# Optimization experiments

Hardware: AMD Instinct MI355X
Metric: run time of the kernel (lower is better)

Reference implementation:

```python
import jax, jax.numpy as jnp
import numpy as np

B, T, L = 256, 512, 40
VOCAB, ED, NC, H = 30000, 8, 22, 64
IN = ED + NC + 1  # GRUCell input: embed + cont + vanco feedback


def setup_inputs():
    key = jax.random.key(0)
    ks = jax.random.split(key, 10)
    cont = jax.random.uniform(ks[0], (B, T, NC), dtype=jnp.float32)
    cat = jax.random.randint(ks[1], (B, T, L), 0, VOCAB, dtype=jnp.int32)
    lb = jax.random.uniform(ks[2], (B, T), dtype=jnp.float32)
    mask = jax.random.randint(ks[3], (B, T), 0, 2, dtype=jnp.int32)
    d = jax.random.uniform(ks[4], (B, T), dtype=jnp.float32)
    td = jax.random.uniform(ks[5], (B, T), dtype=jnp.float32)
    emb = jax.random.normal(ks[6], (VOCAB, ED), dtype=jnp.float32) * 0.1
    emb = emb.at[0].set(0.0)  # padding_idx=0
    W_ih = jax.random.normal(ks[7], (3 * H, IN), dtype=jnp.float32) * 0.1
    W_hh = jax.random.normal(ks[8], (3 * H, H), dtype=jnp.float32) * 0.1
    b_ih = jnp.zeros((3 * H,), jnp.float32)
    b_hh = jnp.zeros((3 * H,), jnp.float32)
    W_out = jax.random.normal(ks[9], (4, H), dtype=jnp.float32) * 0.1
    b_out = jnp.zeros((4,), jnp.float32)
    return dict(cont=cont, cat=cat, lb=lb, mask=mask, d=d, td=td, emb=emb,
                W_ih=W_ih, W_hh=W_hh, b_ih=b_ih, b_hh=b_hh, W_out=W_out, b_out=b_out)


def _forward(cont, cat, lb, mask, d, td, emb, W_ih, W_hh, b_ih, b_hh, W_out, b_out):
    # demographic-derived creatinine clearance, exactly as in the torch code
    age = cont[:, :1, 2] * 16.936469 + 58.239251          # [B,1]
    weight = cont[:, :1, 21] * 30.519849 + 87.5752         # [B,1]
    creat = cont[..., 11] * 1.418099 + 1.314668            # [B,T]
    gender = (cat[:, :1, :] == 5).sum(2).astype(jnp.float32) * 0.15 + 0.85  # [B,1]
    ccl = (140.0 - age) * weight * gender / 72.0 / creat   # [B,T]
    # embedding sum over codes + continuous features
    outEmb = jnp.concatenate([emb[cat].sum(2), cont], axis=2)  # [B,T,ED+NC]
    td24 = td * 24.0
    mf = mask.astype(jnp.float32)
    # step i uses mask/lb of step i-1 for the vanco feedback (0 at i=0)
    mask_prev = jnp.concatenate([jnp.zeros_like(mf[:, :1]), mf[:, :-1]], axis=1)
    lb_prev = jnp.concatenate([jnp.zeros_like(lb[:, :1]), lb[:, :-1]], axis=1)
    Bn = cont.shape[0]

    def step(carry, x):
        h, C, D, A = carry
        e, mp, lp, cc, dd, tt = x
        vfb = jax.lax.stop_gradient(A) * (1.0 - mp) + lp * mp
        xi = jnp.concatenate([e, vfb[:, None]], axis=1)     # [B, IN]
        gi = xi @ W_ih.T + b_ih
        gh = h @ W_hh.T + b_hh
        ir, iz, inn = jnp.split(gi, 3, axis=1)
        hr, hz, hn = jnp.split(gh, 3, axis=1)
        r = jax.nn.sigmoid(ir + hr)
        z = jax.nn.sigmoid(iz + hz)
        n = jnp.tanh(inn + r * hn)
        h = (1.0 - z) * n + z * h                            # GRUCell update
        eta = h @ W_out.T + b_out                            # [B,4]
        e1, e2, e3, e4 = eta[:, 0], eta[:, 1], eta[:, 2], eta[:, 3]
        v1 = 33.1 * jnp.exp(e1)
        k1 = 3.96 * cc / 100.0 * jnp.exp(e2)
        rr = 1000.0 / v1
        v2 = 48.3 * jnp.exp(e4)
        R = -6.99 / 48.3 * jnp.exp(e3)
        k2 = R * v2
        delta = jnp.sqrt((k1 - k2 - R * v1) ** 2 + 4.0 * k1 * R * v1) / v1
        s = (-k1 + k2 + R * v1) / v1
        lam1 = (s - delta) / 2.0
        lam2 = (s + delta) / 2.0
        C1 = rr * (k2 / v1) / lam1 / delta
        C2 = -rr * (k2 / v1) / lam2 / delta
        C3 = -(lam1 - R) / (k2 / v1)
        C4 = -(lam2 - R) / (k2 / v1)
        Cn = ((C + C1) * jnp.exp(lam1 * dd) - C1) * jnp.exp(lam1 * (tt - dd))
        Dn = ((D + C2) * jnp.exp(lam2 * dd) - C2) * jnp.exp(lam2 * (tt - dd))
        An = Cn * C3 + Dn * C4
        return (h, Cn, Dn, An), An

    z0 = jnp.zeros((Bn,), jnp.float32)
    carry0 = (jnp.zeros((Bn, H), jnp.float32), z0, z0, z0)
    xs = (outEmb.transpose(1, 0, 2), mask_prev.T, lb_prev.T, ccl.T, d.T, td24.T)
    _, A_seq = jax.lax.scan(step, carry0, xs)
    return A_seq.T  # [B,T] predicted vancomycin concentration


def reference(cont, cat, lb, mask, d, td, emb, W_ih, W_hh, b_ih, b_hh, W_out, b_out):
    return _forward(cont, cat, lb, mask, d, td, emb, W_ih, W_hh, b_ih, b_hh, W_out, b_out)
```

## Files before the change

kernel.cpp:

```cpp
#include <hip/hip_runtime.h>
#include <math.h>

#define BB 256
#define TT 512
#define LL 40
#define ED 8
#define NC 22
#define HH 64
#define BLK 320

#define L2E 1.4426950408889634f
#define S2E 2.8853900817779268f

__device__ __forceinline__ float fast_rcp(float x)  { return __builtin_amdgcn_rcpf(x); }
__device__ __forceinline__ float fast_exp2(float x) { return __builtin_amdgcn_exp2f(x); }

__device__ __forceinline__ float dpp_add_xor1(float x) {
    int v = __builtin_amdgcn_update_dpp(0, __float_as_int(x), 0xB1, 0xF, 0xF, true);
    return x + __int_as_float(v);
}
__device__ __forceinline__ float dpp_add_xor2(float x) {
    int v = __builtin_amdgcn_update_dpp(0, __float_as_int(x), 0x4E, 0xF, 0xF, true);
    return x + __int_as_float(v);
}
__device__ __forceinline__ float quad_sum(float x) { return dpp_add_xor2(dpp_add_xor1(x)); }

__device__ __forceinline__ float dpp_reduce16(float x) {
    int v;
    v = __builtin_amdgcn_update_dpp(0, __float_as_int(x), 0xB1, 0xF, 0xF, true);  x += __int_as_float(v);
    v = __builtin_amdgcn_update_dpp(0, __float_as_int(x), 0x4E, 0xF, 0xF, true);  x += __int_as_float(v);
    v = __builtin_amdgcn_update_dpp(0, __float_as_int(x), 0x141, 0xF, 0xF, true); x += __int_as_float(v);
    v = __builtin_amdgcn_update_dpp(0, __float_as_int(x), 0x140, 0xF, 0xF, true); x += __int_as_float(v);
    return x;
}

__global__ __launch_bounds__(BLK, 1) void scan_kernel(
    const float* __restrict__ cont, const int* __restrict__ cat,
    const float* __restrict__ lb, const int* __restrict__ mask,
    const float* __restrict__ dvec, const float* __restrict__ td,
    const float* __restrict__ emb,
    const float* __restrict__ W_ih, const float* __restrict__ W_hh,
    const float* __restrict__ b_ih, const float* __restrict__ b_hh,
    const float* __restrict__ W_out, const float* __restrict__ b_out,
    float* __restrict__ out)
{
    const int b   = blockIdx.x;
    const int tid = threadIdx.x;

    __shared__ __align__(128) float  feat[TT * 32];
    __shared__ __align__(16)  float4 sc[TT];
    __shared__ float  cclA[TT];
    __shared__ __align__(128) float hbuf[72];
    __shared__ __align__(16) float out_lds[TT];
    __shared__ float vfb_lds;
    __shared__ float kb_lds;

    const size_t bT    = (size_t)b * TT;
    const int*   catb  = cat  + bT * LL;
    const float* contb = cont + bT * NC;

    const bool isDot = (tid >= 64);
    const int  Ld = tid - 64;
    const int  j  = Ld >> 2;
    const int  q  = Ld & 3;
    const int  ei = tid & 15, ej = tid >> 4;

    float wr_[24], wz_[24], wn_[24];
    float br = 0.f, bz = 0.f, bnx = 0.f, bnh = 0.f;
    float w30r = 0.f, w30z = 0.f, w30n = 0.f;
    float wo0 = 0.f, wo1 = 0.f, wo2 = 0.f, wo3 = 0.f;
    if (isDot) {
        #pragma unroll
        for (int m = 0; m < 24; ++m) {
            const int f = 24 * q + m;
            float a, c, d;
            if (f < 30)      { a = W_ih[j*31+f]; c = W_ih[(j+64)*31+f]; d = W_ih[(j+128)*31+f]; }
            else if (f < 32) { a = 0.f; c = 0.f; d = 0.f; }
            else             { a = W_hh[j*64+f-32]; c = W_hh[(j+64)*64+f-32]; d = W_hh[(j+128)*64+f-32]; }
            wr_[m] = a * L2E;
            wz_[m] = c * L2E;
            wn_[m] = d * S2E;
        }
        #pragma unroll
        for (int m = 0; m < 24; ++m) {
            asm volatile("" : "+v"(wr_[m]));
            asm volatile("" : "+v"(wz_[m]));
            asm volatile("" : "+v"(wn_[m]));
        }
        br   = (b_ih[j]      + b_hh[j])      * L2E;
        bz   = (b_ih[j + 64] + b_hh[j + 64]) * L2E;
        bnx  = b_ih[j + 128] * S2E;
        bnh  = b_hh[j + 128] * S2E;
        w30r = W_ih[j*31 + 30]        * L2E;
        w30z = W_ih[(j+64)*31 + 30]   * L2E;
        w30n = W_ih[(j+128)*31 + 30]  * S2E;
    } else {
        wo0 = W_out[ej * 64 + 4*ei + 0] * L2E;
        wo1 = W_out[ej * 64 + 4*ei + 1] * L2E;
        wo2 = W_out[ej * 64 + 4*ei + 2] * L2E;
        wo3 = W_out[ej * 64 + 4*ei + 3] * L2E;
    }
    const float boL0 = b_out[0] * L2E, boL1 = b_out[1] * L2E;
    const float boL2 = b_out[2] * L2E, boL3 = b_out[3] * L2E;

    for (int i = tid; i < TT * NC; i += BLK) {
        int r = i / NC, c = i - r * NC;
        feat[r * 32 + 8 + c] = contb[i];
    }
    for (int i = tid; i < TT; i += BLK) {
        feat[i * 32 + 30] = 0.f;
        feat[i * 32 + 31] = 0.f;
    }
    for (int i = tid; i < TT * 8; i += BLK) {
        int r = i >> 3, e = i & 7;
        const int* cp = catb + r * LL;
        float acc = 0.f;
        #pragma unroll 8
        for (int l = 0; l < LL; ++l) acc += emb[cp[l] * ED + e];
        feat[r * 32 + e] = acc;
    }
    for (int i = tid; i < TT; i += BLK) {
        float d   = dvec[bT + i];
        float t24 = td[bT + i] * 24.0f;
        sc[i] = make_float4(d * L2E, (t24 - d) * L2E, (float)mask[bT + i], lb[bT + i]);
    }
    if (tid < 72) hbuf[tid] = 0.f;
    if (tid == 0) vfb_lds = 0.f;
    if (tid < 64) {
        int cv = (tid < LL) ? catb[tid] : 0;
        unsigned long long bal = __ballot(tid < LL && cv == 5);
        float g   = (float)__popcll(bal) * 0.15f + 0.85f;
        float age = contb[2]  * 16.936469f + 58.239251f;
        float wgt = contb[21] * 30.519849f + 87.5752f;
        if (tid == 0) kb_lds = (140.0f - age) * wgt * g / 72.0f;
    }
    __syncthreads();
    {
        const float Kb = kb_lds;
        for (int i = tid; i < TT; i += BLK)
            cclA[i] = Kb * fast_rcp(fmaf(contb[i * NC + 11], 1.418099f, 1.314668f));
    }
    __syncthreads();

    float hreg = 0.f;
    float Cc = 0.f, Dc = 0.f;
    float sr = 0.f, sz = 0.f, snx = 0.f, snh = 0.f;
    float4 svc = make_float4(0.f, 0.f, 0.f, 0.f);
    float  ccv = 0.f;

    const float4* hA4 = (const float4*)hbuf;
    const float4* hB4 = (const float4*)(hbuf + 36);

    auto do_dots = [&](int t) {
        const float4* f4t = (const float4*)(feat + t * 32);
        float ra = 0.f, za = 0.f, nxa = 0.f, nha = 0.f;
        #pragma unroll
        for (int k = 0; k < 6; ++k) {
            const int idx = 6 * q + k;
            const float4* pH = (idx < 16) ? (hA4 + (idx - 8)) : (hB4 + (idx - 16));
            const float4* p  = (idx < 8) ? (f4t + idx) : pH;
            const float4 uv = *p;
            ra = fmaf(uv.x, wr_[4*k+0], ra);
            ra = fmaf(uv.y, wr_[4*k+1], ra);
            ra = fmaf(uv.z, wr_[4*k+2], ra);
            ra = fmaf(uv.w, wr_[4*k+3], ra);
            za = fmaf(uv.x, wz_[4*k+0], za);
            za = fmaf(uv.y, wz_[4*k+1], za);
            za = fmaf(uv.z, wz_[4*k+2], za);
            za = fmaf(uv.w, wz_[4*k+3], za);
            if (idx < 8) {
                nxa = fmaf(uv.x, wn_[4*k+0], nxa);
                nxa = fmaf(uv.y, wn_[4*k+1], nxa);
                nxa = fmaf(uv.z, wn_[4*k+2], nxa);
                nxa = fmaf(uv.w, wn_[4*k+3], nxa);
            } else {
                nha = fmaf(uv.x, wn_[4*k+0], nha);
                nha = fmaf(uv.y, wn_[4*k+1], nha);
                nha = fmaf(uv.z, wn_[4*k+2], nha);
                nha = fmaf(uv.w, wn_[4*k+3], nha);
            }
        }
        sr  = quad_sum(ra);
        sz  = quad_sum(za);
        snx = quad_sum(nxa);
        snh = quad_sum(nha);
    };

    if (isDot) do_dots(0);

    for (int t = 0; t < TT; ++t) {
        if (isDot) {
            const float vfb = vfb_lds;
            float prer = sr + br + vfb * w30r;
            float prez = sz + bz + vfb * w30z;
            float r = fast_rcp(1.0f + fast_exp2(-prer));
            float z = fast_rcp(1.0f + fast_exp2(-prez));
            float yp = snx + bnx + vfb * w30n + r * (snh + bnh);
            float n = 1.0f - 2.0f * fast_rcp(fast_exp2(yp) + 1.0f);
            hreg = fmaf(z, hreg - n, n);
            if (q == 0) hbuf[(j < 32) ? j : (36 + j - 32)] = hreg;
        } else {
            svc = sc[t];
            ccv = cclA[t];
        }
        __syncthreads();

        if (isDot) {
            if (t + 1 < TT) do_dots(t + 1);
        } else {
            const float4 hv = (ei < 8) ? hA4[ei] : hB4[ei - 8];
            float p = hv.x * wo0;
            p = fmaf(hv.y, wo1, p);
            p = fmaf(hv.z, wo2, p);
            p = fmaf(hv.w, wo3, p);
            p = dpp_reduce16(p);
            const float e0 = __int_as_float(__builtin_amdgcn_readlane(__float_as_int(p), 0));
            const float e1 = __int_as_float(__builtin_amdgcn_readlane(__float_as_int(p), 16));
            const float e2 = __int_as_float(__builtin_amdgcn_readlane(__float_as_int(p), 32));
            const float e3 = __int_as_float(__builtin_amdgcn_readlane(__float_as_int(p), 48));

            float E1 = fast_exp2(e0 + boL0);
            float E2 = fast_exp2(e1 + boL1);
            float E3 = fast_exp2(e2 + boL2);
            float E4 = fast_exp2(e3 + boL3);
            float v1  = 33.1f * E1;
            float rv1 = fast_rcp(v1);
            float k1  = 0.0396f * ccv * E2;
            float rrr = 1000.0f * rv1;
            float v2  = 48.3f * E4;
            float R   = (-6.99f / 48.3f) * E3;
            float k2  = R * v2;
            float qq  = k1 - k2 - R * v1;
            float disc = fmaf(qq, qq, 4.0f * k1 * R * v1);
            float delta = __builtin_amdgcn_sqrtf(disc) * rv1;
            float sgm  = (k2 - k1 + R * v1) * rv1;
            float lam1 = (sgm - delta) * 0.5f;
            float lam2 = (sgm + delta) * 0.5f;
            float kv  = k2 * rv1;
            float rkv = fast_rcp(kv);
            float C1  = rrr * kv * fast_rcp(lam1 * delta);
            float C2  = -rrr * kv * fast_rcp(lam2 * delta);
            float C3  = -(lam1 - R) * rkv;
            float C4  = -(lam2 - R) * rkv;
            float Cn  = fmaf(Cc + C1, fast_exp2(lam1 * svc.x), -C1) * fast_exp2(lam1 * svc.y);
            float Dn  = fmaf(Dc + C2, fast_exp2(lam2 * svc.x), -C2) * fast_exp2(lam2 * svc.y);
            float An  = fmaf(Cn, C3, Dn * C4);
            Cc = Cn; Dc = Dn;
            if (tid == 0) {
                out_lds[t] = An;
                vfb_lds = fmaf(An, 1.0f - svc.z, svc.w * svc.z);
            }
        }
        __syncthreads();
    }

    if (tid < TT / 4) ((float4*)(out + bT))[tid] = ((const float4*)out_lds)[tid];
}

extern "C" void kernel_launch(void* const* d_in, const int* in_sizes, int n_in,
                              void* d_out, int out_size, void* d_ws, size_t ws_size,
                              hipStream_t stream) {
    const float* cont  = (const float*)d_in[0];
    const int*   cat   = (const int*)  d_in[1];
    const float* lb    = (const float*)d_in[2];
    const int*   mask  = (const int*)  d_in[3];
    const float* dvec  = (const float*)d_in[4];
    const float* td    = (const float*)d_in[5];
    const float* emb   = (const float*)d_in[6];
    const float* W_ih  = (const float*)d_in[7];
    const float* W_hh  = (const float*)d_in[8];
    const float* b_ih  = (const float*)d_in[9];
    const float* b_hh  = (const float*)d_in[10];
    const float* W_out = (const float*)d_in[11];
    const float* b_out = (const float*)d_in[12];
    float* out = (float*)d_out;

    hipLaunchKernelGGL(scan_kernel, dim3(BB), dim3(BLK), 0, stream,
                       cont, cat, lb, mask, dvec, td, emb, W_ih, W_hh, b_ih, b_hh,
                       W_out, b_out, out);
}
```

Before: 476.1 us.

## Split each GRU row dot product across 8 lanes and widen block to 576

```diff
diff --git a/kernel.cpp b/kernel.cpp
--- a/kernel.cpp
+++ b/kernel.cpp
@@ -7,7 +7,7 @@
 #define ED 8
 #define NC 22
 #define HH 64
-#define BLK 320
+#define BLK 576
 
 #define L2E 1.4426950408889634f
 #define S2E 2.8853900817779268f
@@ -23,8 +23,13 @@
     int v = __builtin_amdgcn_update_dpp(0, __float_as_int(x), 0x4E, 0xF, 0xF, true);
     return x + __int_as_float(v);
 }
-__device__ __forceinline__ float quad_sum(float x) { return dpp_add_xor2(dpp_add_xor1(x)); }
-
+__device__ __forceinline__ float dpp_add_mirror8(float x) {
+    int v = __builtin_amdgcn_update_dpp(0, __float_as_int(x), 0x141, 0xF, 0xF, true);
+    return x + __int_as_float(v);
+}
+__device__ __forceinline__ float red8(float x) {
+    return dpp_add_mirror8(dpp_add_xor2(dpp_add_xor1(x)));
+}
 __device__ __forceinline__ float dpp_reduce16(float x) {
     int v;
     v = __builtin_amdgcn_update_dpp(0, __float_as_int(x), 0xB1, 0xF, 0xF, true);  x += __int_as_float(v);
@@ -34,7 +39,7 @@
     return x;
 }
 
-__global__ __launch_bounds__(BLK, 1) void scan_kernel(
+__global__ __launch_bounds__(BLK, 3) void scan_kernel(
     const float* __restrict__ cont, const int* __restrict__ cat,
     const float* __restrict__ lb, const int* __restrict__ mask,
     const float* __restrict__ dvec, const float* __restrict__ td,
@@ -50,8 +55,8 @@
     __shared__ __align__(128) float  feat[TT * 32];
     __shared__ __align__(16)  float4 sc[TT];
     __shared__ float  cclA[TT];
-    __shared__ __align__(128) float hbuf[72];
-    __shared__ __align__(16) float out_lds[TT];
+    __shared__ __align__(16)  float  hbuf[HH];
+    __shared__ __align__(16)  float  out_lds[TT];
     __shared__ float vfb_lds;
     __shared__ float kb_lds;
 
@@ -59,30 +64,36 @@
     const int*   catb  = cat  + bT * LL;
     const float* contb = cont + bT * NC;
 
-    const bool isDot = (tid >= 64);
-    const int  Ld = tid - 64;
-    const int  j  = Ld >> 2;
-    const int  q  = Ld & 3;
-    const int  ei = tid & 15, ej = tid >> 4;
-
-    float wr_[24], wz_[24], wn_[24];
+    const bool isDot = (tid < 512);
+    const int  j  = tid >> 3;
+    const int  s  = tid & 7;
+    const int  l8 = tid - 512;
+    const int  ei = l8 & 15, ej = l8 >> 4;
+
+    float wr_[12], wz_[12], wn_[12];
     float br = 0.f, bz = 0.f, bnx = 0.f, bnh = 0.f;
     float w30r = 0.f, w30z = 0.f, w30n = 0.f;
     float wo0 = 0.f, wo1 = 0.f, wo2 = 0.f, wo3 = 0.f;
     if (isDot) {
+        const int cx0 = 4 * s;
         #pragma unroll
-        for (int m = 0; m < 24; ++m) {
-            const int f = 24 * q + m;
-            float a, c, d;
-            if (f < 30)      { a = W_ih[j*31+f]; c = W_ih[(j+64)*31+f]; d = W_ih[(j+128)*31+f]; }
-            else if (f < 32) { a = 0.f; c = 0.f; d = 0.f; }
-            else             { a = W_hh[j*64+f-32]; c = W_hh[(j+64)*64+f-32]; d = W_hh[(j+128)*64+f-32]; }
-            wr_[m] = a * L2E;
-            wz_[m] = c * L2E;
-            wn_[m] = d * S2E;
+        for (int m = 0; m < 4; ++m) {
+            const int cx = cx0 + m;
+            const float xr = (cx < 30) ? W_ih[j * 31 + cx]         : 0.f;
+            const float xz = (cx < 30) ? W_ih[(j + 64) * 31 + cx]  : 0.f;
+            const float xn = (cx < 30) ? W_ih[(j + 128) * 31 + cx] : 0.f;
+            wr_[m]     = xr * L2E;
+            wz_[m]     = xz * L2E;
+            wn_[m]     = xn * S2E;
+            wr_[4 + m] = W_hh[j * 64 + cx]              * L2E;
+            wz_[4 + m] = W_hh[(j + 64) * 64 + cx]       * L2E;
+            wn_[4 + m] = W_hh[(j + 128) * 64 + cx]      * S2E;
+            wr_[8 + m] = W_hh[j * 64 + 32 + cx]         * L2E;
+            wz_[8 + m] = W_hh[(j + 64) * 64 + 32 + cx]  * L2E;
+            wn_[8 + m] = W_hh[(j + 128) * 64 + 32 + cx] * S2E;
         }
         #pragma unroll
-        for (int m = 0; m < 24; ++m) {
+        for (int m = 0; m < 12; ++m) {
             asm volatile("" : "+v"(wr_[m]));
             asm volatile("" : "+v"(wz_[m]));
             asm volatile("" : "+v"(wn_[m]));
@@ -91,14 +102,14 @@
         bz   = (b_ih[j + 64] + b_hh[j + 64]) * L2E;
         bnx  = b_ih[j + 128] * S2E;
         bnh  = b_hh[j + 128] * S2E;
-        w30r = W_ih[j*31 + 30]        * L2E;
-        w30z = W_ih[(j+64)*31 + 30]   * L2E;
-        w30n = W_ih[(j+128)*31 + 30]  * S2E;
+        w30r = W_ih[j * 31 + 30]         * L2E;
+        w30z = W_ih[(j + 64) * 31 + 30]  * L2E;
+        w30n = W_ih[(j + 128) * 31 + 30] * S2E;
     } else {
-        wo0 = W_out[ej * 64 + 4*ei + 0] * L2E;
-        wo1 = W_out[ej * 64 + 4*ei + 1] * L2E;
-        wo2 = W_out[ej * 64 + 4*ei + 2] * L2E;
-        wo3 = W_out[ej * 64 + 4*ei + 3] * L2E;
+        wo0 = W_out[ej * 64 + 4 * ei + 0] * L2E;
+        wo1 = W_out[ej * 64 + 4 * ei + 1] * L2E;
+        wo2 = W_out[ej * 64 + 4 * ei + 2] * L2E;
+        wo3 = W_out[ej * 64 + 4 * ei + 3] * L2E;
     }
     const float boL0 = b_out[0] * L2E, boL1 = b_out[1] * L2E;
     const float boL2 = b_out[2] * L2E, boL3 = b_out[3] * L2E;
@@ -111,20 +122,23 @@
         feat[i * 32 + 30] = 0.f;
         feat[i * 32 + 31] = 0.f;
     }
-    for (int i = tid; i < TT * 8; i += BLK) {
-        int r = i >> 3, e = i & 7;
+    for (int i = tid; i < TT * 2; i += BLK) {
+        int r = i >> 1, qd = i & 1;
         const int* cp = catb + r * LL;
-        float acc = 0.f;
+        float4 acc = make_float4(0.f, 0.f, 0.f, 0.f);
         #pragma unroll 8
-        for (int l = 0; l < LL; ++l) acc += emb[cp[l] * ED + e];
-        feat[r * 32 + e] = acc;
+        for (int l = 0; l < LL; ++l) {
+            const float4 ev = *((const float4*)(emb + cp[l] * ED) + qd);
+            acc.x += ev.x; acc.y += ev.y; acc.z += ev.z; acc.w += ev.w;
+        }
+        ((float4*)feat)[r * 8 + qd] = acc;
     }
     for (int i = tid; i < TT; i += BLK) {
         float d   = dvec[bT + i];
         float t24 = td[bT + i] * 24.0f;
         sc[i] = make_float4(d * L2E, (t24 - d) * L2E, (float)mask[bT + i], lb[bT + i]);
     }
-    if (tid < 72) hbuf[tid] = 0.f;
+    if (tid < HH) hbuf[tid] = 0.f;
     if (tid == 0) vfb_lds = 0.f;
     if (tid < 64) {
         int cv = (tid < LL) ? catb[tid] : 0;
@@ -148,42 +162,53 @@
     float4 svc = make_float4(0.f, 0.f, 0.f, 0.f);
     float  ccv = 0.f;
 
-    const float4* hA4 = (const float4*)hbuf;
-    const float4* hB4 = (const float4*)(hbuf + 36);
+    const float4* hbuf4 = (const float4*)hbuf;
 
     auto do_dots = [&](int t) {
-        const float4* f4t = (const float4*)(feat + t * 32);
-        float ra = 0.f, za = 0.f, nxa = 0.f, nha = 0.f;
-        #pragma unroll
-        for (int k = 0; k < 6; ++k) {
-            const int idx = 6 * q + k;
-            const float4* pH = (idx < 16) ? (hA4 + (idx - 8)) : (hB4 + (idx - 16));
-            const float4* p  = (idx < 8) ? (f4t + idx) : pH;
-            const float4 uv = *p;
-            ra = fmaf(uv.x, wr_[4*k+0], ra);
-            ra = fmaf(uv.y, wr_[4*k+1], ra);
-            ra = fmaf(uv.z, wr_[4*k+2], ra);
-            ra = fmaf(uv.w, wr_[4*k+3], ra);
-            za = fmaf(uv.x, wz_[4*k+0], za);
-            za = fmaf(uv.y, wz_[4*k+1], za);
-            za = fmaf(uv.z, wz_[4*k+2], za);
-            za = fmaf(uv.w, wz_[4*k+3], za);
-            if (idx < 8) {
-                nxa = fmaf(uv.x, wn_[4*k+0], nxa);
-                nxa = fmaf(uv.y, wn_[4*k+1], nxa);
-                nxa = fmaf(uv.z, wn_[4*k+2], nxa);
-                nxa = fmaf(uv.w, wn_[4*k+3], nxa);
-            } else {
-                nha = fmaf(uv.x, wn_[4*k+0], nha);
-                nha = fmaf(uv.y, wn_[4*k+1], nha);
-                nha = fmaf(uv.z, wn_[4*k+2], nha);
-                nha = fmaf(uv.w, wn_[4*k+3], nha);
-            }
-        }
-        sr  = quad_sum(ra);
-        sz  = quad_sum(za);
-        snx = quad_sum(nxa);
-        snh = quad_sum(nha);
+        const float4 u0 = ((const float4*)(feat + t * 32))[s];
+        const float4 u1 = hbuf4[s];
+        const float4 u2 = hbuf4[s + 8];
+        float ra, za, nxa, nha;
+        ra  = u0.x * wr_[0];
+        ra  = fmaf(u0.y, wr_[1],  ra);
+        ra  = fmaf(u0.z, wr_[2],  ra);
+        ra  = fmaf(u0.w, wr_[3],  ra);
+        ra  = fmaf(u1.x, wr_[4],  ra);
+        ra  = fmaf(u1.y, wr_[5],  ra);
+        ra  = fmaf(u1.z, wr_[6],  ra);
+        ra  = fmaf(u1.w, wr_[7],  ra);
+        ra  = fmaf(u2.x, wr_[8],  ra);
+        ra  = fmaf(u2.y, wr_[9],  ra);
+        ra  = fmaf(u2.z, wr_[10], ra);
+        ra  = fmaf(u2.w, wr_[11], ra);
+        za  = u0.x * wz_[0];
+        za  = fmaf(u0.y, wz_[1],  za);
+        za  = fmaf(u0.z, wz_[2],  za);
+        za  = fmaf(u0.w, wz_[3],  za);
+        za  = fmaf(u1.x, wz_[4],  za);
+        za  = fmaf(u1.y, wz_[5],  za);
+        za  = fmaf(u1.z, wz_[6],  za);
+        za  = fmaf(u1.w, wz_[7],  za);
+        za  = fmaf(u2.x, wz_[8],  za);
+        za  = fmaf(u2.y, wz_[9],  za);
+        za  = fmaf(u2.z, wz_[10], za);
+        za  = fmaf(u2.w, wz_[11], za);
+        nxa = u0.x * wn_[0];
+        nxa = fmaf(u0.y, wn_[1],  nxa);
+        nxa = fmaf(u0.z, wn_[2],  nxa);
+        nxa = fmaf(u0.w, wn_[3],  nxa);
+        nha = u1.x * wn_[4];
+        nha = fmaf(u1.y, wn_[5],  nha);
+        nha = fmaf(u1.z, wn_[6],  nha);
+        nha = fmaf(u1.w, wn_[7],  nha);
+        nha = fmaf(u2.x, wn_[8],  nha);
+        nha = fmaf(u2.y, wn_[9],  nha);
+        nha = fmaf(u2.z, wn_[10], nha);
+        nha = fmaf(u2.w, wn_[11], nha);
+        sr  = red8(ra);
+        sz  = red8(za);
+        snx = red8(nxa);
+        snh = red8(nha);
     };
 
     if (isDot) do_dots(0);
@@ -198,7 +223,7 @@
             float yp = snx + bnx + vfb * w30n + r * (snh + bnh);
             float n = 1.0f - 2.0f * fast_rcp(fast_exp2(yp) + 1.0f);
             hreg = fmaf(z, hreg - n, n);
-            if (q == 0) hbuf[(j < 32) ? j : (36 + j - 32)] = hreg;
+            if (s == 0) hbuf[j] = hreg;
         } else {
             svc = sc[t];
             ccv = cclA[t];
@@ -208,7 +233,7 @@
         if (isDot) {
             if (t + 1 < TT) do_dots(t + 1);
         } else {
-            const float4 hv = (ei < 8) ? hA4[ei] : hB4[ei - 8];
+            const float4 hv = hbuf4[ei];
             float p = hv.x * wo0;
             p = fmaf(hv.y, wo1, p);
             p = fmaf(hv.z, wo2, p);
@@ -246,7 +271,7 @@
             float Dn  = fmaf(Dc + C2, fast_exp2(lam2 * svc.x), -C2) * fast_exp2(lam2 * svc.y);
             float An  = fmaf(Cn, C3, Dn * C4);
             Cc = Cn; Dc = Dn;
-            if (tid == 0) {
+            if (tid == 512) {
                 out_lds[t] = An;
                 vfb_lds = fmaf(An, 1.0f - svc.z, svc.w * svc.z);
             }
```

Result: faster. 425.5 us (-10.6%).

## Fold PK head into every wave, double-buffer hidden state, one barrier per step

Applied to the files above, without the earlier changes.

```diff
diff --git a/kernel.cpp b/kernel.cpp
--- a/kernel.cpp
+++ b/kernel.cpp
@@ -7,7 +7,7 @@
 #define ED 8
 #define NC 22
 #define HH 64
-#define BLK 320
+#define BLK 256
 
 #define L2E 1.4426950408889634f
 #define S2E 2.8853900817779268f
@@ -24,17 +24,21 @@
     return x + __int_as_float(v);
 }
 __device__ __forceinline__ float quad_sum(float x) { return dpp_add_xor2(dpp_add_xor1(x)); }
-
-__device__ __forceinline__ float dpp_reduce16(float x) {
+__device__ __forceinline__ float wave_sum(float x) {
     int v;
     v = __builtin_amdgcn_update_dpp(0, __float_as_int(x), 0xB1, 0xF, 0xF, true);  x += __int_as_float(v);
     v = __builtin_amdgcn_update_dpp(0, __float_as_int(x), 0x4E, 0xF, 0xF, true);  x += __int_as_float(v);
     v = __builtin_amdgcn_update_dpp(0, __float_as_int(x), 0x141, 0xF, 0xF, true); x += __int_as_float(v);
     v = __builtin_amdgcn_update_dpp(0, __float_as_int(x), 0x140, 0xF, 0xF, true); x += __int_as_float(v);
+    x += __shfl_xor(x, 16);
+    x += __shfl_xor(x, 32);
     return x;
 }
 
-__global__ __launch_bounds__(BLK, 1) void scan_kernel(
+__global__
+__attribute__((amdgpu_flat_work_group_size(BLK, BLK)))
+__attribute__((amdgpu_waves_per_eu(1, 1)))
+void scan_kernel(
     const float* __restrict__ cont, const int* __restrict__ cat,
     const float* __restrict__ lb, const int* __restrict__ mask,
     const float* __restrict__ dvec, const float* __restrict__ td,
@@ -44,62 +48,53 @@
     const float* __restrict__ W_out, const float* __restrict__ b_out,
     float* __restrict__ out)
 {
-    const int b   = blockIdx.x;
-    const int tid = threadIdx.x;
+    const int b    = blockIdx.x;
+    const int tid  = threadIdx.x;
+    const int lane = tid & 63;
 
     __shared__ __align__(128) float  feat[TT * 32];
     __shared__ __align__(16)  float4 sc[TT];
     __shared__ float  cclA[TT];
-    __shared__ __align__(128) float hbuf[72];
-    __shared__ __align__(16) float out_lds[TT];
-    __shared__ float vfb_lds;
+    __shared__ __align__(128) float  hbuf[2][HH];
+    __shared__ __align__(16)  float  out_lds[TT];
     __shared__ float kb_lds;
 
     const size_t bT    = (size_t)b * TT;
     const int*   catb  = cat  + bT * LL;
     const float* contb = cont + bT * NC;
 
-    const bool isDot = (tid >= 64);
-    const int  Ld = tid - 64;
-    const int  j  = Ld >> 2;
-    const int  q  = Ld & 3;
-    const int  ei = tid & 15, ej = tid >> 4;
+    const int j = tid >> 2;
+    const int s = tid & 3;
 
     float wr_[24], wz_[24], wn_[24];
-    float br = 0.f, bz = 0.f, bnx = 0.f, bnh = 0.f;
-    float w30r = 0.f, w30z = 0.f, w30n = 0.f;
-    float wo0 = 0.f, wo1 = 0.f, wo2 = 0.f, wo3 = 0.f;
-    if (isDot) {
-        #pragma unroll
-        for (int m = 0; m < 24; ++m) {
-            const int f = 24 * q + m;
-            float a, c, d;
-            if (f < 30)      { a = W_ih[j*31+f]; c = W_ih[(j+64)*31+f]; d = W_ih[(j+128)*31+f]; }
-            else if (f < 32) { a = 0.f; c = 0.f; d = 0.f; }
-            else             { a = W_hh[j*64+f-32]; c = W_hh[(j+64)*64+f-32]; d = W_hh[(j+128)*64+f-32]; }
-            wr_[m] = a * L2E;
-            wz_[m] = c * L2E;
-            wn_[m] = d * S2E;
-        }
-        #pragma unroll
-        for (int m = 0; m < 24; ++m) {
-            asm volatile("" : "+v"(wr_[m]));
-            asm volatile("" : "+v"(wz_[m]));
-            asm volatile("" : "+v"(wn_[m]));
-        }
-        br   = (b_ih[j]      + b_hh[j])      * L2E;
-        bz   = (b_ih[j + 64] + b_hh[j + 64]) * L2E;
-        bnx  = b_ih[j + 128] * S2E;
-        bnh  = b_hh[j + 128] * S2E;
-        w30r = W_ih[j*31 + 30]        * L2E;
-        w30z = W_ih[(j+64)*31 + 30]   * L2E;
-        w30n = W_ih[(j+128)*31 + 30]  * S2E;
-    } else {
-        wo0 = W_out[ej * 64 + 4*ei + 0] * L2E;
-        wo1 = W_out[ej * 64 + 4*ei + 1] * L2E;
-        wo2 = W_out[ej * 64 + 4*ei + 2] * L2E;
-        wo3 = W_out[ej * 64 + 4*ei + 3] * L2E;
-    }
+    #pragma unroll
+    for (int m = 0; m < 24; ++m) {
+        const int f = 24 * s + m;
+        float a, c, d;
+        if (f < 30)      { a = W_ih[j*31+f]; c = W_ih[(j+64)*31+f]; d = W_ih[(j+128)*31+f]; }
+        else if (f < 32) { a = 0.f; c = 0.f; d = 0.f; }
+        else             { a = W_hh[j*64+f-32]; c = W_hh[(j+64)*64+f-32]; d = W_hh[(j+128)*64+f-32]; }
+        wr_[m] = a * L2E;
+        wz_[m] = c * L2E;
+        wn_[m] = d * S2E;
+    }
+    #pragma unroll
+    for (int m = 0; m < 24; ++m) {
+        asm volatile("" : "+v"(wr_[m]));
+        asm volatile("" : "+v"(wz_[m]));
+        asm volatile("" : "+v"(wn_[m]));
+    }
+    const float br   = (b_ih[j]      + b_hh[j])      * L2E;
+    const float bz   = (b_ih[j + 64] + b_hh[j + 64]) * L2E;
+    const float bnx  = b_ih[j + 128] * S2E;
+    const float bnh  = b_hh[j + 128] * S2E;
+    const float w30r = W_ih[j * 31 + 30]         * L2E;
+    const float w30z = W_ih[(j + 64) * 31 + 30]  * L2E;
+    const float w30n = W_ih[(j + 128) * 31 + 30] * S2E;
+    const float wo0 = W_out[0 * HH + lane];
+    const float wo1 = W_out[1 * HH + lane];
+    const float wo2 = W_out[2 * HH + lane];
+    const float wo3 = W_out[3 * HH + lane];
     const float boL0 = b_out[0] * L2E, boL1 = b_out[1] * L2E;
     const float boL2 = b_out[2] * L2E, boL3 = b_out[3] * L2E;
 
@@ -111,21 +106,23 @@
         feat[i * 32 + 30] = 0.f;
         feat[i * 32 + 31] = 0.f;
     }
-    for (int i = tid; i < TT * 8; i += BLK) {
-        int r = i >> 3, e = i & 7;
+    for (int i = tid; i < TT * 2; i += BLK) {
+        int r = i >> 1, qd = i & 1;
         const int* cp = catb + r * LL;
-        float acc = 0.f;
+        float4 acc = make_float4(0.f, 0.f, 0.f, 0.f);
         #pragma unroll 8
-        for (int l = 0; l < LL; ++l) acc += emb[cp[l] * ED + e];
-        feat[r * 32 + e] = acc;
+        for (int l = 0; l < LL; ++l) {
+            const float4 ev = *((const float4*)(emb + cp[l] * ED) + qd);
+            acc.x += ev.x; acc.y += ev.y; acc.z += ev.z; acc.w += ev.w;
+        }
+        ((float4*)feat)[r * 8 + qd] = acc;
     }
     for (int i = tid; i < TT; i += BLK) {
         float d   = dvec[bT + i];
         float t24 = td[bT + i] * 24.0f;
         sc[i] = make_float4(d * L2E, (t24 - d) * L2E, (float)mask[bT + i], lb[bT + i]);
     }
-    if (tid < 72) hbuf[tid] = 0.f;
-    if (tid == 0) vfb_lds = 0.f;
+    if (tid < HH) { hbuf[0][tid] = 0.f; hbuf[1][tid] = 0.f; }
     if (tid < 64) {
         int cv = (tid < LL) ? catb[tid] : 0;
         unsigned long long bal = __ballot(tid < LL && cv == 5);
@@ -140,26 +137,21 @@
         for (int i = tid; i < TT; i += BLK)
             cclA[i] = Kb * fast_rcp(fmaf(contb[i * NC + 11], 1.418099f, 1.314668f));
     }
-    __syncthreads();
 
     float hreg = 0.f;
-    float Cc = 0.f, Dc = 0.f;
+    float vfb  = 0.f;
+    float S    = 0.f;
+    const float sgnC = (lane & 1) ? -1.f : 1.f;
     float sr = 0.f, sz = 0.f, snx = 0.f, snh = 0.f;
-    float4 svc = make_float4(0.f, 0.f, 0.f, 0.f);
-    float  ccv = 0.f;
-
-    const float4* hA4 = (const float4*)hbuf;
-    const float4* hB4 = (const float4*)(hbuf + 36);
-
-    auto do_dots = [&](int t) {
+
+    auto do_dots = [&](int t, const float* hb) {
         const float4* f4t = (const float4*)(feat + t * 32);
+        const float4* hb4 = (const float4*)hb;
         float ra = 0.f, za = 0.f, nxa = 0.f, nha = 0.f;
         #pragma unroll
         for (int k = 0; k < 6; ++k) {
-            const int idx = 6 * q + k;
-            const float4* pH = (idx < 16) ? (hA4 + (idx - 8)) : (hB4 + (idx - 16));
-            const float4* p  = (idx < 8) ? (f4t + idx) : pH;
-            const float4 uv = *p;
+            const int idx = 6 * s + k;
+            const float4 uv = (idx < 8) ? f4t[idx] : hb4[idx - 8];
             ra = fmaf(uv.x, wr_[4*k+0], ra);
             ra = fmaf(uv.y, wr_[4*k+1], ra);
             ra = fmaf(uv.z, wr_[4*k+2], ra);
@@ -186,11 +178,11 @@
         snh = quad_sum(nha);
     };
 
-    if (isDot) do_dots(0);
+    do_dots(0, hbuf[1]);
+    __syncthreads();
 
     for (int t = 0; t < TT; ++t) {
-        if (isDot) {
-            const float vfb = vfb_lds;
+        {
             float prer = sr + br + vfb * w30r;
             float prez = sz + bz + vfb * w30z;
             float r = fast_rcp(1.0f + fast_exp2(-prer));
@@ -198,62 +190,52 @@
             float yp = snx + bnx + vfb * w30n + r * (snh + bnh);
             float n = 1.0f - 2.0f * fast_rcp(fast_exp2(yp) + 1.0f);
             hreg = fmaf(z, hreg - n, n);
-            if (q == 0) hbuf[(j < 32) ? j : (36 + j - 32)] = hreg;
-        } else {
-            svc = sc[t];
-            ccv = cclA[t];
+            if (s == 0) hbuf[t & 1][j] = hreg;
         }
         __syncthreads();
 
-        if (isDot) {
-            if (t + 1 < TT) do_dots(t + 1);
-        } else {
-            const float4 hv = (ei < 8) ? hA4[ei] : hB4[ei - 8];
-            float p = hv.x * wo0;
-            p = fmaf(hv.y, wo1, p);
-            p = fmaf(hv.z, wo2, p);
-            p = fmaf(hv.w, wo3, p);
-            p = dpp_reduce16(p);
-            const float e0 = __int_as_float(__builtin_amdgcn_readlane(__float_as_int(p), 0));
-            const float e1 = __int_as_float(__builtin_amdgcn_readlane(__float_as_int(p), 16));
-            const float e2 = __int_as_float(__builtin_amdgcn_readlane(__float_as_int(p), 32));
-            const float e3 = __int_as_float(__builtin_amdgcn_readlane(__float_as_int(p), 48));
-
-            float E1 = fast_exp2(e0 + boL0);
-            float E2 = fast_exp2(e1 + boL1);
-            float E3 = fast_exp2(e2 + boL2);
-            float E4 = fast_exp2(e3 + boL3);
-            float v1  = 33.1f * E1;
-            float rv1 = fast_rcp(v1);
-            float k1  = 0.0396f * ccv * E2;
-            float rrr = 1000.0f * rv1;
-            float v2  = 48.3f * E4;
-            float R   = (-6.99f / 48.3f) * E3;
-            float k2  = R * v2;
-            float qq  = k1 - k2 - R * v1;
-            float disc = fmaf(qq, qq, 4.0f * k1 * R * v1);
-            float delta = __builtin_amdgcn_sqrtf(disc) * rv1;
-            float sgm  = (k2 - k1 + R * v1) * rv1;
-            float lam1 = (sgm - delta) * 0.5f;
-            float lam2 = (sgm + delta) * 0.5f;
-            float kv  = k2 * rv1;
-            float rkv = fast_rcp(kv);
-            float C1  = rrr * kv * fast_rcp(lam1 * delta);
-            float C2  = -rrr * kv * fast_rcp(lam2 * delta);
-            float C3  = -(lam1 - R) * rkv;
-            float C4  = -(lam2 - R) * rkv;
-            float Cn  = fmaf(Cc + C1, fast_exp2(lam1 * svc.x), -C1) * fast_exp2(lam1 * svc.y);
-            float Dn  = fmaf(Dc + C2, fast_exp2(lam2 * svc.x), -C2) * fast_exp2(lam2 * svc.y);
-            float An  = fmaf(Cn, C3, Dn * C4);
-            Cc = Cn; Dc = Dn;
-            if (tid == 0) {
-                out_lds[t] = An;
-                vfb_lds = fmaf(An, 1.0f - svc.z, svc.w * svc.z);
-            }
-        }
-        __syncthreads();
-    }
-
+        const float* hb = hbuf[t & 1];
+
+        const int tn = (t + 1 < TT) ? (t + 1) : t;
+        do_dots(tn, hb);
+
+        const float hv = hb[lane];
+        const float e0 = wave_sum(hv * wo0);
+        const float e1 = wave_sum(hv * wo1);
+        const float e2 = wave_sum(hv * wo2);
+        const float e3 = wave_sum(hv * wo3);
+
+        const float4 sv = sc[t];
+        const float  cc = cclA[t];
+        float E1 = fast_exp2(e0 * L2E + boL0);
+        float E2 = fast_exp2(e1 * L2E + boL1);
+        float E3 = fast_exp2(e2 * L2E + boL2);
+        float E4 = fast_exp2(e3 * L2E + boL3);
+        float v1  = 33.1f * E1;
+        float rv1 = fast_rcp(v1);
+        float k1  = 0.0396f * cc * E2;
+        float rrr = 1000.0f * rv1;
+        float v2  = 48.3f * E4;
+        float R   = (-6.99f / 48.3f) * E3;
+        float k2  = R * v2;
+        float qq  = k1 - k2 - R * v1;
+        float disc = fmaf(qq, qq, 4.0f * k1 * R * v1);
+        float delta = __builtin_amdgcn_sqrtf(disc) * rv1;
+        float sgm  = (k2 - k1 + R * v1) * rv1;
+        float sd   = (lane & 1) ? delta : -delta;
+        float lam  = (sgm + sd) * 0.5f;
+        float kv   = k2 * rv1;
+        float rkv  = fast_rcp(kv);
+        float Cs   = sgnC * rrr * kv * fast_rcp(lam * delta);
+        float Snew = fmaf(S + Cs, fast_exp2(lam * sv.x), -Cs) * fast_exp2(lam * sv.y);
+        float contrib = Snew * (-(lam - R) * rkv);
+        float An = dpp_add_xor1(contrib);
+        S = Snew;
+        vfb = fmaf(An, 1.0f - sv.z, sv.w * sv.z);
+        if (tid == 0) out_lds[t] = An;
+    }
+
+    __syncthreads();
     if (tid < TT / 4) ((float4*)(out + bT))[tid] = ((const float4*)out_lds)[tid];
 }
 
```

Result: slower. 560.1 us (+17.7%).
